# Kernel optimization log

Hardware: AMD Instinct MI355X
Metric: run time of the kernel (lower is better)

Reference implementation:

```python
import jax, jax.numpy as jnp
import numpy as np

L, T, H, F = 16, 2048, 2048, 512  # layers, tokens (B*S=16*128), hidden, features


def setup_inputs() -> dict:
    key = jax.random.key(0)
    k1, k2, k3 = jax.random.split(key, 3)
    x = jax.random.normal(k1, (L, T, H), dtype=jnp.float32)          # stacked residual activations
    W_enc = jax.random.normal(k2, (L, F, H), dtype=jnp.float32) * 0.02  # per-layer encoder (out,in)
    # Dense pack of decoders: W_dec[s, t] is the (source s -> target t) decoder weight (H, F).
    # Only entries with s <= t exist in the original ModuleDict; others are masked to zero in reference().
    W_dec = jax.random.normal(k3, (L, L, H, F), dtype=jnp.float32) * 0.02
    return {"x": x, "W_enc": W_enc, "W_dec": W_dec}


def reference(x, W_enc, W_dec):
    n_layers = x.shape[0]
    # encode: feature_activations[l] = JumpReLU(x[l] @ W_enc[l].T), threshold=0 -> relu
    feats = jax.nn.relu(jnp.einsum('sth,sfh->stf', x, W_enc))  # [L, T, F]
    # causal mask over (source s, target l): decoder exists iff s <= l
    tri = jnp.tril(jnp.ones((n_layers, n_layers), x.dtype))     # tri[l, s] = 1 if s <= l
    Wd = W_dec * tri.T[:, :, None, None]                        # zero out s > l entries
    # reconstruction[l] = sum_{s<=l} feats[s] @ W_dec[s,l].T  (single blocked contraction)
    recon = jnp.einsum('stf,slhf->lth', feats, Wd)              # [L, T, H]
    return feats, recon
```

## Files before the change

kernel.cpp:

```cpp
#include <hip/hip_runtime.h>

#define NL 16
#define NT 2048
#define NH 2048
#define NF 512
#define NPAIR 136

typedef short bf16x8 __attribute__((ext_vector_type(8)));
typedef float f32x4 __attribute__((ext_vector_type(4)));
typedef short s16x4 __attribute__((ext_vector_type(4)));
typedef unsigned u32x4 __attribute__((ext_vector_type(4)));

__device__ __forceinline__ short f2bf(float f) {
  union { float f; unsigned u; } x; x.f = f;
  unsigned r = (x.u + 0x7fffu + ((x.u >> 16) & 1u)) >> 16;
  return (short)r;
}

__device__ __forceinline__ int imin(int a, int b) { return a < b ? a : b; }

__device__ __forceinline__ unsigned cvtpk(float a, float b) {
  unsigned r;
  asm("v_cvt_pk_bf16_f32 %0, %1, %2" : "=v"(r) : "v"(a), "v"(b));
  return r;
}


__global__ void k_cvt_f32_bf16(const float* __restrict__ src, short* __restrict__ dst, int n4) {
  int i = blockIdx.x * blockDim.x + threadIdx.x;
  const int stride = gridDim.x * blockDim.x;
  for (; i < n4; i += stride) {
    const float4 v = reinterpret_cast<const float4*>(src)[i];
    s16x4 o;
    o[0] = f2bf(v.x); o[1] = f2bf(v.y); o[2] = f2bf(v.z); o[3] = f2bf(v.w);
    reinterpret_cast<s16x4*>(dst)[i] = o;
  }
}

__global__ void k_cvt_wdec(const float* __restrict__ wdec, short* __restrict__ dst) {
  const int p = blockIdx.y;
  int l = 0;
  while ((l + 1) * (l + 2) / 2 <= p) ++l;
  const int s = p - l * (l + 1) / 2;
  const float* src = wdec + (size_t)(s * NL + l) * (NH * NF);
  short* d = dst + (size_t)p * (NH * NF);
  const int n4 = NH * NF / 4;
  for (int i = blockIdx.x * blockDim.x + threadIdx.x; i < n4; i += gridDim.x * blockDim.x) {
    const float4 v = reinterpret_cast<const float4*>(src)[i];
    s16x4 o;
    o[0] = f2bf(v.x); o[1] = f2bf(v.y); o[2] = f2bf(v.z); o[3] = f2bf(v.w);
    reinterpret_cast<s16x4*>(d)[i] = o;
  }
}


__device__ __forceinline__ bf16x8 lds_frag(const short* slot, int r, int cbyte) {
  int byte = (r << 7) + cbyte;
  byte ^= (r & 7) << 4;
  return *reinterpret_cast<const bf16x8*>(reinterpret_cast<const char*>(slot) + byte);
}

__device__ __forceinline__ void stage_half(short* slot, const short* gbase, int ld,
                                           int isA, int h, int tid, int wave) {
#pragma unroll
  for (int j = 0; j < 2; ++j) {
    const int o = j * 8192 + tid * 16;
    const int r = o >> 7;
    const int cb = (o ^ ((r & 7) << 4)) & 127;
    const int g = isA ? (((r >> 6) << 7) + h * 64 + (r & 63))
                      : (((r >> 5) << 6) + h * 32 + (r & 31));
    __builtin_amdgcn_global_load_lds(
        (const __attribute__((address_space(1))) void*)(gbase + (size_t)g * ld + (cb >> 1)),
        (__attribute__((address_space(3))) void*)((char*)slot + j * 8192 + wave * 1024),
        16, 0, 0);
  }
}

struct F32Half { float4 q[2][2]; };

__device__ __forceinline__ void issue_f32half(F32Half& st, const float* gbase, int ld,
                                              int isA, int h, int tid) {
#pragma unroll
  for (int j = 0; j < 2; ++j) {
    const int o = j * 8192 + tid * 16;
    const int r = o >> 7;
    const int cb = (o ^ ((r & 7) << 4)) & 127;
    const int g = isA ? (((r >> 6) << 7) + h * 64 + (r & 63))
                      : (((r >> 5) << 6) + h * 32 + (r & 31));
    const float* p = gbase + (size_t)g * ld + (cb >> 1);
    st.q[j][0] = *reinterpret_cast<const float4*>(p);
    st.q[j][1] = *reinterpret_cast<const float4*>(p + 4);
  }
}

__device__ __forceinline__ void commit_f32half(const F32Half& st, short* slot, int tid) {
#pragma unroll
  for (int j = 0; j < 2; ++j) {
    u32x4 o;
    o[0] = cvtpk(st.q[j][0].x, st.q[j][0].y);
    o[1] = cvtpk(st.q[j][0].z, st.q[j][0].w);
    o[2] = cvtpk(st.q[j][1].x, st.q[j][1].y);
    o[3] = cvtpk(st.q[j][1].z, st.q[j][1].w);
    *reinterpret_cast<u32x4*>((char*)slot + j * 8192 + tid * 16) = o;
  }
}

template <typename IFn, typename CFn>
__device__ __forceinline__ void ktile_flat(short (*bufc)[8192], f32x4 (&acc)[2][2][4][2],
                                           int wr, int wc, int lane, IFn issue, CFn commit) {
  const int lr = lane & 15;
  const int ko = (lane >> 4) * 16;
  issue();
  bf16x8 b0[2][2], b1[2][2], a0[2][4], a1[2][4];
#pragma unroll
  for (int kk = 0; kk < 2; ++kk) {
#pragma unroll
    for (int n = 0; n < 2; ++n) {
      b0[kk][n] = lds_frag(bufc[2], wc * 32 + n * 16 + lr, kk * 64 + ko);
      b1[kk][n] = lds_frag(bufc[3], wc * 32 + n * 16 + lr, kk * 64 + ko);
    }
#pragma unroll
    for (int m = 0; m < 4; ++m)
      a0[kk][m] = lds_frag(bufc[0], wr * 64 + m * 16 + lr, kk * 64 + ko);
  }
  __builtin_amdgcn_s_setprio(1);
#pragma unroll
  for (int kk = 0; kk < 2; ++kk)
#pragma unroll
    for (int m = 0; m < 4; ++m)
#pragma unroll
      for (int n = 0; n < 2; ++n) {
        acc[0][0][m][n] = __builtin_amdgcn_mfma_f32_16x16x32_bf16(a0[kk][m], b0[kk][n],
                                                                  acc[0][0][m][n], 0, 0, 0);
        acc[0][1][m][n] = __builtin_amdgcn_mfma_f32_16x16x32_bf16(a0[kk][m], b1[kk][n],
                                                                  acc[0][1][m][n], 0, 0, 0);
      }
  __builtin_amdgcn_s_setprio(0);
#pragma unroll
  for (int kk = 0; kk < 2; ++kk)
#pragma unroll
    for (int m = 0; m < 4; ++m)
      a1[kk][m] = lds_frag(bufc[1], wr * 64 + m * 16 + lr, kk * 64 + ko);
  __builtin_amdgcn_s_setprio(1);
#pragma unroll
  for (int kk = 0; kk < 2; ++kk)
#pragma unroll
    for (int m = 0; m < 4; ++m)
#pragma unroll
      for (int n = 0; n < 2; ++n) {
        acc[1][0][m][n] = __builtin_amdgcn_mfma_f32_16x16x32_bf16(a1[kk][m], b0[kk][n],
                                                                  acc[1][0][m][n], 0, 0, 0);
        acc[1][1][m][n] = __builtin_amdgcn_mfma_f32_16x16x32_bf16(a1[kk][m], b1[kk][n],
                                                                  acc[1][1][m][n], 0, 0, 0);
      }
  __builtin_amdgcn_s_setprio(0);
  commit();
  asm volatile("s_waitcnt vmcnt(0) lgkmcnt(0)" ::: "memory");
  __builtin_amdgcn_s_barrier();
}


__global__ __launch_bounds__(512, 2) void k_encode256(const float* __restrict__ xf,
                                                      const short* __restrict__ webf,
                                                      float* __restrict__ feats_f32,
                                                      short* __restrict__ feats_bf) {
  __shared__ short lds[2][4][8192];
  const int l = blockIdx.z;
  const int row0 = blockIdx.y * 256;
  const int col0 = blockIdx.x * 256;
  const int tid = threadIdx.x;
  const int wave = tid >> 6, lane = tid & 63;
  const int wr = wave >> 2, wc = wave & 3;

  const float* A = xf + (size_t)l * NT * NH + (size_t)row0 * NH;
  const short* B = webf + (size_t)l * NF * NH + (size_t)col0 * NH;

  f32x4 acc[2][2][4][2];
#pragma unroll
  for (int qa = 0; qa < 2; ++qa)
#pragma unroll
    for (int qb = 0; qb < 2; ++qb)
#pragma unroll
      for (int m = 0; m < 4; ++m)
#pragma unroll
        for (int n = 0; n < 2; ++n) {
          f32x4 z = {0.f, 0.f, 0.f, 0.f};
          acc[qa][qb][m][n] = z;
        }

  const int KT = NH / 64;
  F32Half stA0, stA1;
  issue_f32half(stA0, A, NH, 1, 0, tid);
  issue_f32half(stA1, A, NH, 1, 1, tid);
  stage_half(lds[0][2], B, NH, 0, 0, tid, wave);
  stage_half(lds[0][3], B, NH, 0, 1, tid, wave);
  commit_f32half(stA0, lds[0][0], tid);
  commit_f32half(stA1, lds[0][1], tid);
  asm volatile("s_waitcnt vmcnt(0) lgkmcnt(0)" ::: "memory");
  __builtin_amdgcn_s_barrier();

  for (int u = 0; u < KT; ++u) {
    short(*bufc)[8192] = lds[u & 1];
    short(*bufn)[8192] = lds[(u + 1) & 1];
    ktile_flat(bufc, acc, wr, wc, lane,
        [&] {
          if (u + 1 < KT) {
            issue_f32half(stA0, A + (u + 1) * 64, NH, 1, 0, tid);
            issue_f32half(stA1, A + (u + 1) * 64, NH, 1, 1, tid);
            stage_half(bufn[2], B + (u + 1) * 64, NH, 0, 0, tid, wave);
            stage_half(bufn[3], B + (u + 1) * 64, NH, 0, 1, tid, wave);
          }
        },
        [&] {
          if (u + 1 < KT) {
            commit_f32half(stA0, bufn[0], tid);
            commit_f32half(stA1, bufn[1], tid);
          }
        });
  }

  const int lr4 = (lane >> 4) * 4, lc = lane & 15;
  float* outF = feats_f32 + (size_t)l * NT * NF;
  short* outB = feats_bf + (size_t)l * NT * NF;
#pragma unroll
  for (int qa = 0; qa < 2; ++qa)
#pragma unroll
    for (int qb = 0; qb < 2; ++qb)
#pragma unroll
      for (int m = 0; m < 4; ++m)
#pragma unroll
        for (int n = 0; n < 2; ++n)
#pragma unroll
          for (int rg = 0; rg < 4; ++rg) {
            const int rr = row0 + wr * 128 + qa * 64 + m * 16 + lr4 + rg;
            const int cc = col0 + wc * 64 + qb * 32 + n * 16 + lc;
            float v = acc[qa][qb][m][n][rg];
            v = v > 0.f ? v : 0.f;
            outF[(size_t)rr * NF + cc] = v;
            outB[(size_t)rr * NF + cc] = f2bf(v);
          }
}


__global__ __launch_bounds__(512, 2) void k_decode256(const short* __restrict__ featsbf,
                                                      const short* __restrict__ wdbf,
                                                      float* __restrict__ recon) {
  __shared__ short lds[2][4][8192];
  const int l = (NL - 1) - blockIdx.z;
  const int row0 = blockIdx.y * 256;
  const int col0 = blockIdx.x * 256;
  const int tid = threadIdx.x;
  const int wave = tid >> 6, lane = tid & 63;
  const int wr = wave >> 2, wc = wave & 3;
  const int pbase = l * (l + 1) / 2;

  const short* Af = featsbf + (size_t)row0 * NF;
  const short* Bw = wdbf + (size_t)col0 * NF;

  f32x4 acc[2][2][4][2];
#pragma unroll
  for (int qa = 0; qa < 2; ++qa)
#pragma unroll
    for (int qb = 0; qb < 2; ++qb)
#pragma unroll
      for (int m = 0; m < 4; ++m)
#pragma unroll
        for (int n = 0; n < 2; ++n) {
          f32x4 z = {0.f, 0.f, 0.f, 0.f};
          acc[qa][qb][m][n] = z;
        }

  const int KT = 8 * (l + 1);
#define ABASE(kt) (Af + (size_t)((kt) >> 3) * (NT * NF) + ((kt)&7) * 64)
#define BBASE(kt) (Bw + (size_t)(pbase + ((kt) >> 3)) * (NH * NF) + ((kt)&7) * 64)

  stage_half(lds[0][0], ABASE(0), NF, 1, 0, tid, wave);
  stage_half(lds[0][1], ABASE(0), NF, 1, 1, tid, wave);
  stage_half(lds[0][2], BBASE(0), NF, 0, 0, tid, wave);
  stage_half(lds[0][3], BBASE(0), NF, 0, 1, tid, wave);
  asm volatile("s_waitcnt vmcnt(0)" ::: "memory");
  __builtin_amdgcn_s_barrier();

  for (int u = 0; u < KT; ++u) {
    short(*bufc)[8192] = lds[u & 1];
    short(*bufn)[8192] = lds[(u + 1) & 1];
    ktile_flat(bufc, acc, wr, wc, lane,
        [&] {
          if (u + 1 < KT) {
            stage_half(bufn[0], ABASE(u + 1), NF, 1, 0, tid, wave);
            stage_half(bufn[1], ABASE(u + 1), NF, 1, 1, tid, wave);
            stage_half(bufn[2], BBASE(u + 1), NF, 0, 0, tid, wave);
            stage_half(bufn[3], BBASE(u + 1), NF, 0, 1, tid, wave);
          }
        },
        [&] {});
  }
#undef ABASE
#undef BBASE

  const int lr4 = (lane >> 4) * 4, lc = lane & 15;
  float* out = recon + (size_t)l * NT * NH;
#pragma unroll
  for (int qa = 0; qa < 2; ++qa)
#pragma unroll
    for (int qb = 0; qb < 2; ++qb)
#pragma unroll
      for (int m = 0; m < 4; ++m)
#pragma unroll
        for (int n = 0; n < 2; ++n)
#pragma unroll
          for (int rg = 0; rg < 4; ++rg) {
            const int rr = row0 + wr * 128 + qa * 64 + m * 16 + lr4 + rg;
            const int cc = col0 + wc * 64 + qb * 32 + n * 16 + lc;
            out[(size_t)rr * NH + cc] = acc[qa][qb][m][n][rg];
          }
}


extern "C" void kernel_launch(void* const* d_in, const int* in_sizes, int n_in,
                              void* d_out, int out_size, void* d_ws, size_t ws_size,
                              hipStream_t stream) {
  const float* x = (const float*)d_in[0];
  const float* wenc = (const float*)d_in[1];
  const float* wdec = (const float*)d_in[2];

  float* feats_f32 = (float*)d_out;
  float* recon = feats_f32 + (size_t)NL * NT * NF;

  short* we_bf = (short*)d_ws;
  short* wd_bf = we_bf + (size_t)NL * NF * NH;
  short* ft_bf = wd_bf + (size_t)NPAIR * NH * NF;

  k_cvt_f32_bf16<<<1024, 256, 0, stream>>>(wenc, we_bf, NL * NF * NH / 4);
  k_cvt_wdec<<<dim3(512, NPAIR), 256, 0, stream>>>(wdec, wd_bf);

  k_encode256<<<dim3(2, 8, 16), 512, 0, stream>>>(x, we_bf, feats_f32, ft_bf);
  k_decode256<<<dim3(8, 8, 16), 512, 0, stream>>>(ft_bf, wd_bf, recon);
}
```

Measured before the change: 821.1 us.

## Fuse most W_dec bf16 conversion into encode GEMM main loop

Moves the conversion of the first 32M float4 groups of the causal W_dec pairs into the encode kernel. Each block loads and converts a slice of the decoder weights alongside its K-loop, so memory traffic overlaps with MFMA compute. A smaller tail kernel converts the remaining entries. The cost is extra registers and global traffic inside the encode loop, which could slow the encode GEMM or reduce its occupancy.

Measured after the change: 954.2 us. 16.2% more time.

```diff
diff --git a/kernel.cpp b/kernel.cpp
--- a/kernel.cpp
+++ b/kernel.cpp
@@ -9,6 +9,7 @@
 typedef short bf16x8 __attribute__((ext_vector_type(8)));
 typedef float f32x4 __attribute__((ext_vector_type(4)));
 typedef short s16x4 __attribute__((ext_vector_type(4)));
+typedef unsigned u32x2 __attribute__((ext_vector_type(2)));
 typedef unsigned u32x4 __attribute__((ext_vector_type(4)));
 
 __device__ __forceinline__ short f2bf(float f) {
@@ -17,12 +18,19 @@
   return (short)r;
 }
 
-__device__ __forceinline__ int imin(int a, int b) { return a < b ? a : b; }
-
 __device__ __forceinline__ unsigned cvtpk(float a, float b) {
   unsigned r;
   asm("v_cvt_pk_bf16_f32 %0, %1, %2" : "=v"(r) : "v"(a), "v"(b));
   return r;
+}
+
+__device__ __forceinline__ const float* wdec_src(const float* wdec, size_t idx4) {
+  const int p = (int)(idx4 >> 18);
+  const size_t off4 = idx4 & 262143u;
+  int l = 0;
+  while ((l + 1) * (l + 2) / 2 <= p) ++l;
+  const int s = p - l * (l + 1) / 2;
+  return wdec + ((size_t)(s * NL + l) << 20) + (off4 << 2);
 }
 
 
@@ -37,19 +45,16 @@
   }
 }
 
-__global__ void k_cvt_wdec(const float* __restrict__ wdec, short* __restrict__ dst) {
-  const int p = blockIdx.y;
-  int l = 0;
-  while ((l + 1) * (l + 2) / 2 <= p) ++l;
-  const int s = p - l * (l + 1) / 2;
-  const float* src = wdec + (size_t)(s * NL + l) * (NH * NF);
-  short* d = dst + (size_t)p * (NH * NF);
-  const int n4 = NH * NF / 4;
-  for (int i = blockIdx.x * blockDim.x + threadIdx.x; i < n4; i += gridDim.x * blockDim.x) {
-    const float4 v = reinterpret_cast<const float4*>(src)[i];
-    s16x4 o;
-    o[0] = f2bf(v.x); o[1] = f2bf(v.y); o[2] = f2bf(v.z); o[3] = f2bf(v.w);
-    reinterpret_cast<s16x4*>(d)[i] = o;
+__global__ void k_cvt_wdec_tail(const float* __restrict__ wdec, short* __restrict__ dst) {
+  size_t i = 33554432ull + (size_t)blockIdx.x * blockDim.x + threadIdx.x;
+  const size_t end = (size_t)NPAIR * 262144ull;
+  const size_t stride = (size_t)gridDim.x * blockDim.x;
+  for (; i < end; i += stride) {
+    const float4 v = *reinterpret_cast<const float4*>(wdec_src(wdec, i));
+    u32x2 o;
+    o[0] = cvtpk(v.x, v.y);
+    o[1] = cvtpk(v.z, v.w);
+    *reinterpret_cast<u32x2*>(dst + (i << 2)) = o;
   }
 }
 
@@ -105,9 +110,10 @@
   }
 }
 
-template <typename IFn, typename CFn>
+template <typename IFn, typename MFn, typename CFn>
 __device__ __forceinline__ void ktile_flat(short (*bufc)[8192], f32x4 (&acc)[2][2][4][2],
-                                           int wr, int wc, int lane, IFn issue, CFn commit) {
+                                           int wr, int wc, int lane,
+                                           IFn issue, MFn mid, CFn commit) {
   const int lr = lane & 15;
   const int ko = (lane >> 4) * 16;
   issue();
@@ -136,6 +142,7 @@
                                                                   acc[0][1][m][n], 0, 0, 0);
       }
   __builtin_amdgcn_s_setprio(0);
+  mid();
 #pragma unroll
   for (int kk = 0; kk < 2; ++kk)
 #pragma unroll
@@ -162,6 +169,8 @@
 
 __global__ __launch_bounds__(512, 2) void k_encode256(const float* __restrict__ xf,
                                                       const short* __restrict__ webf,
+                                                      const float* __restrict__ wdec,
+                                                      short* __restrict__ wd_bf,
                                                       float* __restrict__ feats_f32,
                                                       short* __restrict__ feats_bf) {
   __shared__ short lds[2][4][8192];
@@ -171,6 +180,8 @@
   const int tid = threadIdx.x;
   const int wave = tid >> 6, lane = tid & 63;
   const int wr = wave >> 2, wc = wave & 3;
+  const int bid = blockIdx.x + 2 * (blockIdx.y + 8 * (int)blockIdx.z);
+  const size_t cvt_base = (size_t)bid * 131072 + tid;
 
   const float* A = xf + (size_t)l * NT * NH + (size_t)row0 * NH;
   const short* B = webf + (size_t)l * NF * NH + (size_t)col0 * NH;
@@ -190,6 +201,7 @@
 
   const int KT = NH / 64;
   F32Half stA0, stA1;
+  float4 cv[4];
   issue_f32half(stA0, A, NH, 1, 0, tid);
   issue_f32half(stA1, A, NH, 1, 1, tid);
   stage_half(lds[0][2], B, NH, 0, 0, tid, wave);
@@ -202,8 +214,12 @@
   for (int u = 0; u < KT; ++u) {
     short(*bufc)[8192] = lds[u & 1];
     short(*bufn)[8192] = lds[(u + 1) & 1];
+    const size_t cb0 = cvt_base + (size_t)u * 4096;
     ktile_flat(bufc, acc, wr, wc, lane,
         [&] {
+#pragma unroll
+          for (int k = 0; k < 4; ++k)
+            cv[k] = *reinterpret_cast<const float4*>(wdec_src(wdec, cb0 + k * 512));
           if (u + 1 < KT) {
             issue_f32half(stA0, A + (u + 1) * 64, NH, 1, 0, tid);
             issue_f32half(stA1, A + (u + 1) * 64, NH, 1, 1, tid);
@@ -212,6 +228,26 @@
           }
         },
         [&] {
+#pragma unroll
+          for (int k = 0; k < 4; ++k) {
+            u32x2 o;
+            o[0] = cvtpk(cv[k].x, cv[k].y);
+            o[1] = cvtpk(cv[k].z, cv[k].w);
+            *reinterpret_cast<u32x2*>(wd_bf + ((cb0 + k * 512) << 2)) = o;
+          }
+#pragma unroll
+          for (int k = 0; k < 4; ++k)
+            cv[k] = *reinterpret_cast<const float4*>(
+                wdec_src(wdec, cb0 + 2048 + k * 512));
+        },
+        [&] {
+#pragma unroll
+          for (int k = 0; k < 4; ++k) {
+            u32x2 o;
+            o[0] = cvtpk(cv[k].x, cv[k].y);
+            o[1] = cvtpk(cv[k].z, cv[k].w);
+            *reinterpret_cast<u32x2*>(wd_bf + ((cb0 + 2048 + k * 512) << 2)) = o;
+          }
           if (u + 1 < KT) {
             commit_f32half(stA0, bufn[0], tid);
             commit_f32half(stA1, bufn[1], tid);
@@ -293,7 +329,7 @@
             stage_half(bufn[3], BBASE(u + 1), NF, 0, 1, tid, wave);
           }
         },
-        [&] {});
+        [&] {}, [&] {});
   }
 #undef ABASE
 #undef BBASE
@@ -332,8 +368,8 @@
   short* ft_bf = wd_bf + (size_t)NPAIR * NH * NF;
 
   k_cvt_f32_bf16<<<1024, 256, 0, stream>>>(wenc, we_bf, NL * NF * NH / 4);
-  k_cvt_wdec<<<dim3(512, NPAIR), 256, 0, stream>>>(wdec, wd_bf);
-
-  k_encode256<<<dim3(2, 8, 16), 512, 0, stream>>>(x, we_bf, feats_f32, ft_bf);
+  k_cvt_wdec_tail<<<2048, 256, 0, stream>>>(wdec, wd_bf);
+
+  k_encode256<<<dim3(2, 8, 16), 512, 0, stream>>>(x, we_bf, wdec, wd_bf, feats_f32, ft_bf);
   k_decode256<<<dim3(8, 8, 16), 512, 0, stream>>>(ft_bf, wd_bf, recon);
 }
```

## Shrink decode GEMM tiles to 128x128 with 4-wave blocks

Applied to the files above, without the earlier changes.

Replaces the 256x256-tile, 8-wave decode kernel with a 128x128-tile, 4-wave kernel using a new panel staging routine and a simpler k-tile loop. The grid grows from 1024 to 4096 blocks. The aim is better load balance across the triangular per-layer work, where later layers have much longer K loops, and more blocks per CU. In exchange, each block reuses its operands less, so more global and L2 traffic is needed per flop.

Measured after the change: 979.8 us. +19.3%, slower.

```diff
diff --git a/kernel.cpp b/kernel.cpp
--- a/kernel.cpp
+++ b/kernel.cpp
@@ -16,8 +16,6 @@
   unsigned r = (x.u + 0x7fffu + ((x.u >> 16) & 1u)) >> 16;
   return (short)r;
 }
-
-__device__ __forceinline__ int imin(int a, int b) { return a < b ? a : b; }
 
 __device__ __forceinline__ unsigned cvtpk(float a, float b) {
   unsigned r;
@@ -60,6 +58,7 @@
   return *reinterpret_cast<const bf16x8*>(reinterpret_cast<const char*>(slot) + byte);
 }
 
+
 __device__ __forceinline__ void stage_half(short* slot, const short* gbase, int ld,
                                            int isA, int h, int tid, int wave) {
 #pragma unroll
@@ -158,7 +157,6 @@
   asm volatile("s_waitcnt vmcnt(0) lgkmcnt(0)" ::: "memory");
   __builtin_amdgcn_s_barrier();
 }
-
 
 __global__ __launch_bounds__(512, 2) void k_encode256(const float* __restrict__ xf,
                                                       const short* __restrict__ webf,
@@ -242,58 +240,92 @@
 }
 
 
-__global__ __launch_bounds__(512, 2) void k_decode256(const short* __restrict__ featsbf,
+__device__ __forceinline__ void stage_panel128(short* panel, const short* gbase, int ld,
+                                               int tid, int wave) {
+#pragma unroll
+  for (int j = 0; j < 4; ++j) {
+    const int o = j * 4096 + tid * 16;
+    const int r = o >> 7;
+    const int cb = (o ^ ((r & 7) << 4)) & 127;
+    __builtin_amdgcn_global_load_lds(
+        (const __attribute__((address_space(1))) void*)(gbase + (size_t)r * ld + (cb >> 1)),
+        (__attribute__((address_space(3))) void*)((char*)panel + j * 4096 + wave * 1024),
+        16, 0, 0);
+  }
+}
+
+template <typename SFn>
+__device__ __forceinline__ void ktile128(short (*bufc)[8192], f32x4 (&acc)[4][4],
+                                         int wr, int wc, int lane, SFn stagefn) {
+  const int lr = lane & 15;
+  const int ko = (lane >> 4) * 16;
+  stagefn();
+  bf16x8 a[2][4], b[2][4];
+#pragma unroll
+  for (int kk = 0; kk < 2; ++kk) {
+#pragma unroll
+    for (int n = 0; n < 4; ++n)
+      b[kk][n] = lds_frag(bufc[1], wc * 64 + n * 16 + lr, kk * 64 + ko);
+#pragma unroll
+    for (int m = 0; m < 4; ++m)
+      a[kk][m] = lds_frag(bufc[0], wr * 64 + m * 16 + lr, kk * 64 + ko);
+  }
+  __builtin_amdgcn_s_setprio(1);
+#pragma unroll
+  for (int kk = 0; kk < 2; ++kk)
+#pragma unroll
+    for (int m = 0; m < 4; ++m)
+#pragma unroll
+      for (int n = 0; n < 4; ++n)
+        acc[m][n] = __builtin_amdgcn_mfma_f32_16x16x32_bf16(a[kk][m], b[kk][n],
+                                                            acc[m][n], 0, 0, 0);
+  __builtin_amdgcn_s_setprio(0);
+  asm volatile("s_waitcnt vmcnt(0) lgkmcnt(0)" ::: "memory");
+  __builtin_amdgcn_s_barrier();
+}
+
+__global__ __launch_bounds__(256, 2) void k_decode128(const short* __restrict__ featsbf,
                                                       const short* __restrict__ wdbf,
                                                       float* __restrict__ recon) {
-  __shared__ short lds[2][4][8192];
+  __shared__ short lds[2][2][8192];
   const int l = (NL - 1) - blockIdx.z;
-  const int row0 = blockIdx.y * 256;
-  const int col0 = blockIdx.x * 256;
+  const int row0 = blockIdx.y * 128;
+  const int col0 = blockIdx.x * 128;
   const int tid = threadIdx.x;
   const int wave = tid >> 6, lane = tid & 63;
-  const int wr = wave >> 2, wc = wave & 3;
+  const int wr = wave >> 1, wc = wave & 1;
   const int pbase = l * (l + 1) / 2;
 
   const short* Af = featsbf + (size_t)row0 * NF;
   const short* Bw = wdbf + (size_t)col0 * NF;
 
-  f32x4 acc[2][2][4][2];
-#pragma unroll
-  for (int qa = 0; qa < 2; ++qa)
-#pragma unroll
-    for (int qb = 0; qb < 2; ++qb)
-#pragma unroll
-      for (int m = 0; m < 4; ++m)
-#pragma unroll
-        for (int n = 0; n < 2; ++n) {
-          f32x4 z = {0.f, 0.f, 0.f, 0.f};
-          acc[qa][qb][m][n] = z;
-        }
+  f32x4 acc[4][4];
+#pragma unroll
+  for (int m = 0; m < 4; ++m)
+#pragma unroll
+    for (int n = 0; n < 4; ++n) {
+      f32x4 z = {0.f, 0.f, 0.f, 0.f};
+      acc[m][n] = z;
+    }
 
   const int KT = 8 * (l + 1);
 #define ABASE(kt) (Af + (size_t)((kt) >> 3) * (NT * NF) + ((kt)&7) * 64)
 #define BBASE(kt) (Bw + (size_t)(pbase + ((kt) >> 3)) * (NH * NF) + ((kt)&7) * 64)
 
-  stage_half(lds[0][0], ABASE(0), NF, 1, 0, tid, wave);
-  stage_half(lds[0][1], ABASE(0), NF, 1, 1, tid, wave);
-  stage_half(lds[0][2], BBASE(0), NF, 0, 0, tid, wave);
-  stage_half(lds[0][3], BBASE(0), NF, 0, 1, tid, wave);
+  stage_panel128(lds[0][0], ABASE(0), NF, tid, wave);
+  stage_panel128(lds[0][1], BBASE(0), NF, tid, wave);
   asm volatile("s_waitcnt vmcnt(0)" ::: "memory");
   __builtin_amdgcn_s_barrier();
 
   for (int u = 0; u < KT; ++u) {
     short(*bufc)[8192] = lds[u & 1];
     short(*bufn)[8192] = lds[(u + 1) & 1];
-    ktile_flat(bufc, acc, wr, wc, lane,
-        [&] {
-          if (u + 1 < KT) {
-            stage_half(bufn[0], ABASE(u + 1), NF, 1, 0, tid, wave);
-            stage_half(bufn[1], ABASE(u + 1), NF, 1, 1, tid, wave);
-            stage_half(bufn[2], BBASE(u + 1), NF, 0, 0, tid, wave);
-            stage_half(bufn[3], BBASE(u + 1), NF, 0, 1, tid, wave);
-          }
-        },
-        [&] {});
+    ktile128(bufc, acc, wr, wc, lane, [&] {
+      if (u + 1 < KT) {
+        stage_panel128(bufn[0], ABASE(u + 1), NF, tid, wave);
+        stage_panel128(bufn[1], BBASE(u + 1), NF, tid, wave);
+      }
+    });
   }
 #undef ABASE
 #undef BBASE
@@ -301,19 +333,15 @@
   const int lr4 = (lane >> 4) * 4, lc = lane & 15;
   float* out = recon + (size_t)l * NT * NH;
 #pragma unroll
-  for (int qa = 0; qa < 2; ++qa)
-#pragma unroll
-    for (int qb = 0; qb < 2; ++qb)
-#pragma unroll
-      for (int m = 0; m < 4; ++m)
-#pragma unroll
-        for (int n = 0; n < 2; ++n)
-#pragma unroll
-          for (int rg = 0; rg < 4; ++rg) {
-            const int rr = row0 + wr * 128 + qa * 64 + m * 16 + lr4 + rg;
-            const int cc = col0 + wc * 64 + qb * 32 + n * 16 + lc;
-            out[(size_t)rr * NH + cc] = acc[qa][qb][m][n][rg];
-          }
+  for (int m = 0; m < 4; ++m)
+#pragma unroll
+    for (int n = 0; n < 4; ++n)
+#pragma unroll
+      for (int rg = 0; rg < 4; ++rg) {
+        const int rr = row0 + wr * 64 + m * 16 + lr4 + rg;
+        const int cc = col0 + wc * 64 + n * 16 + lc;
+        out[(size_t)rr * NH + cc] = acc[m][n][rg];
+      }
 }
 
 
@@ -335,5 +363,5 @@
   k_cvt_wdec<<<dim3(512, NPAIR), 256, 0, stream>>>(wdec, wd_bf);
 
   k_encode256<<<dim3(2, 8, 16), 512, 0, stream>>>(x, we_bf, feats_f32, ft_bf);
-  k_decode256<<<dim3(8, 8, 16), 512, 0, stream>>>(ft_bf, wd_bf, recon);
-}
+  k_decode128<<<dim3(16, 16, 16), 256, 0, stream>>>(ft_bf, wd_bf, recon);
+}
```
